# Performance work log

Measured on AMD Instinct MI355X. Metric: run time of the kernel, lower is better.

The kernel has to match this reference:

```python
import jax, jax.numpy as jnp
import numpy as np

D_MODEL = 512
H = 8
D_K = D_MODEL // H


def setup_inputs() -> dict:
    key = jax.random.key(0)
    ks = jax.random.split(key, 11)
    B, S = 2, 4096
    s = 1.0 / np.sqrt(D_MODEL)
    return {
        "q": jax.random.normal(ks[0], (B, S, D_MODEL), jnp.float32),
        "k": jax.random.normal(ks[1], (B, S, D_MODEL), jnp.float32),
        "v": jax.random.normal(ks[2], (B, S, D_MODEL), jnp.float32),
        "w_q": jax.random.normal(ks[3], (D_MODEL, D_MODEL), jnp.float32) * s,
        "b_q": jax.random.normal(ks[4], (D_MODEL,), jnp.float32) * 0.01,
        "w_k": jax.random.normal(ks[5], (D_MODEL, D_MODEL), jnp.float32) * s,
        "b_k": jax.random.normal(ks[6], (D_MODEL,), jnp.float32) * 0.01,
        "w_v": jax.random.normal(ks[7], (D_MODEL, D_MODEL), jnp.float32) * s,
        "b_v": jax.random.normal(ks[8], (D_MODEL,), jnp.float32) * 0.01,
        "w_o": jax.random.normal(ks[9], (D_MODEL, D_MODEL), jnp.float32) * s,
        "b_o": jax.random.normal(ks[10], (D_MODEL,), jnp.float32) * 0.01,
    }


def reference(q, k, v, w_q, b_q, w_k, b_k, w_v, b_v, w_o, b_o):
    B, S, _ = q.shape
    # QKV projections (torch Linear: x @ W.T + b)
    query = q @ w_q.T + b_q
    key_ = k @ w_k.T + b_k
    value = v @ w_v.T + b_v
    # split heads -> [B, H, S, D_K]
    qh = query.reshape(B, S, H, D_K).transpose(0, 2, 1, 3)
    kh = key_.reshape(B, S, H, D_K).transpose(0, 2, 1, 3)
    vh = value.reshape(B, S, H, D_K).transpose(0, 2, 1, 3)
    scores = jnp.einsum('bhsd,bhtd->bhst', qh, kh) / jnp.sqrt(
        jnp.asarray(D_K, qh.dtype))
    attn = jax.nn.softmax(scores, axis=-1)  # dropout = identity in eval
    ctx = jnp.einsum('bhst,bhtd->bhsd', attn, vh)
    out = ctx.transpose(0, 2, 1, 3).reshape(B, S, H * D_K)
    return out @ w_o.T + b_o
```

## Files before the change

### kernel.cpp

```cpp
#include <hip/hip_runtime.h>
#include <hip/hip_bf16.h>


typedef __bf16 bf16_t;
typedef __bf16 bf16x8 __attribute__((ext_vector_type(8)));
typedef __bf16 bf16x4 __attribute__((ext_vector_type(4)));
typedef float f32x4 __attribute__((ext_vector_type(4)));

#define S_LEN 4096
#define NH 8
#define DK 64
#define DMODEL 512
#define NB 2
#define KVB 64
#define QB 128

#define EXP2F(x) __builtin_amdgcn_exp2f(x)

__device__ inline void gload_lds16(const void* g, void* l) {
  __builtin_amdgcn_global_load_lds(
      (const __attribute__((address_space(1))) unsigned int*)g,
      (__attribute__((address_space(3))) unsigned int*)l, 16, 0, 0);
}

__global__ __launch_bounds__(256) void cvt3(
    const float* __restrict__ q, const float* __restrict__ k,
    const float* __restrict__ v, bf16_t* __restrict__ x0,
    bf16_t* __restrict__ x1, bf16_t* __restrict__ x2)
{
  const int z = blockIdx.x >> 11;
  const float* src = z == 0 ? q : z == 1 ? k : v;
  bf16_t* dst = z == 0 ? x0 : z == 1 ? x1 : x2;
  const int i = ((blockIdx.x & 2047) * 256 + threadIdx.x) * 8;
  f32x4 a = *reinterpret_cast<const f32x4*>(src + i);
  f32x4 b = *reinterpret_cast<const f32x4*>(src + i + 4);
  bf16x8 r;
#pragma unroll
  for (int j = 0; j < 4; ++j) { r[j] = (__bf16)a[j]; r[j + 4] = (__bf16)b[j]; }
  *reinterpret_cast<bf16x8*>(dst + i) = r;
}

__global__ __launch_bounds__(256) void cvt_weights(
    const float* __restrict__ w0, const float* __restrict__ w1,
    const float* __restrict__ w2, const float* __restrict__ w3,
    bf16_t* __restrict__ o0, bf16_t* __restrict__ o1,
    bf16_t* __restrict__ o2, bf16_t* __restrict__ o3)
{
  const float* src = blockIdx.y == 0 ? w0 : blockIdx.y == 1 ? w1
                   : blockIdx.y == 2 ? w2 : w3;
  bf16_t* dst = blockIdx.y == 0 ? o0 : blockIdx.y == 1 ? o1
              : blockIdx.y == 2 ? o2 : o3;
  const int i = (blockIdx.x * 256 + threadIdx.x) * 4;
  f32x4 v = *reinterpret_cast<const f32x4*>(src + i);
  bf16x4 r;
#pragma unroll
  for (int j = 0; j < 4; ++j) r[j] = (__bf16)v[j];
  *reinterpret_cast<bf16x4*>(dst + i) = r;
}

template <typename TO, bool FUSED>
__global__ __launch_bounds__(256) void gemm_tile(
    const bf16_t* __restrict__ A0, const bf16_t* __restrict__ W0,
    const float* __restrict__ bb0, TO* __restrict__ oo0,
    const bf16_t* __restrict__ A1, const bf16_t* __restrict__ W1,
    const float* __restrict__ bb1, TO* __restrict__ oo1,
    int mode_last)
{
  const bf16_t* A; const bf16_t* W; const float* bias; TO* out; int mode;
  if (FUSED) {
    if (blockIdx.z == 0) { A = A0; W = W0; bias = bb0; out = oo0; }
    else                 { A = A1; W = W1; bias = bb1; out = oo1; }
    mode = 0;
  } else { A = A0; W = W0; bias = bb0; out = oo0; mode = mode_last; }

  const int mtile = blockIdx.x * 128;
  const int ntile = blockIdx.y * 64;
  const int wave = threadIdx.x >> 6;
  const int lane = threadIdx.x & 63;
  const int l16 = lane & 15;
  const int g = lane >> 4;

  __shared__ bf16_t ldsA[2][128][64];
  __shared__ bf16_t ldsB[2][64][64];

  const int srow8 = 8 * wave + (lane >> 3);
  const int sslot = (lane & 7) ^ ((lane >> 3) & 7);
  const char* Asrc = (const char*)A + ((size_t)(mtile + srow8) * DMODEL) * 2 + sslot * 16;
  const char* Bsrc = (const char*)W + ((size_t)(ntile + srow8) * DMODEL) * 2 + sslot * 16;
  const size_t rblk = (size_t)32 * DMODEL * 2;

  f32x4 acc[2][4];
#pragma unroll
  for (int mb = 0; mb < 2; ++mb)
#pragma unroll
    for (int nb = 0; nb < 4; ++nb) acc[mb][nb] = (f32x4){0.f, 0.f, 0.f, 0.f};

  const int rxor = (l16 & 7) << 4;

#pragma unroll
  for (int c = 0; c < 4; ++c)
    gload_lds16(Asrc + c * rblk, (char*)&ldsA[0][c * 32 + 8 * wave][0]);
#pragma unroll
  for (int c = 0; c < 2; ++c)
    gload_lds16(Bsrc + c * rblk, (char*)&ldsB[0][c * 32 + 8 * wave][0]);
  __syncthreads();

  const int NSTEP = DMODEL / 64;
  int buf = 0;
  for (int t = 0; t < NSTEP; ++t) {
    if (t + 1 < NSTEP) {
      const size_t ko = (size_t)(t + 1) * 128;
#pragma unroll
      for (int c = 0; c < 4; ++c)
        gload_lds16(Asrc + c * rblk + ko, (char*)&ldsA[buf ^ 1][c * 32 + 8 * wave][0]);
#pragma unroll
      for (int c = 0; c < 2; ++c)
        gload_lds16(Bsrc + c * rblk + ko, (char*)&ldsB[buf ^ 1][c * 32 + 8 * wave][0]);
    }

#pragma unroll
    for (int ks = 0; ks < 2; ++ks) {
      bf16x8 af[2];
#pragma unroll
      for (int mb = 0; mb < 2; ++mb) {
        const int arow = wave * 32 + mb * 16 + l16;
        af[mb] = *reinterpret_cast<const bf16x8*>(
            (const char*)&ldsA[buf][0][0] + arow * 128 + ((ks * 64 + g * 16) ^ rxor));
      }
#pragma unroll
      for (int nb = 0; nb < 4; ++nb) {
        const int brow = nb * 16 + l16;
        bf16x8 bfr = *reinterpret_cast<const bf16x8*>(
            (const char*)&ldsB[buf][0][0] + brow * 128 + ((ks * 64 + g * 16) ^ rxor));
#pragma unroll
        for (int mb = 0; mb < 2; ++mb)
          acc[mb][nb] = __builtin_amdgcn_mfma_f32_16x16x32_bf16(af[mb], bfr, acc[mb][nb], 0, 0, 0);
      }
    }

    __syncthreads();
    buf ^= 1;
  }

#pragma unroll
  for (int mb = 0; mb < 2; ++mb) {
    const int m0 = mtile + wave * 32 + mb * 16;
#pragma unroll
    for (int nb = 0; nb < 4; ++nb) {
      const int n = ntile + nb * 16 + l16;
      const float bv = bias[n];
#pragma unroll
      for (int r = 0; r < 4; ++r) {
        const int m = m0 + g * 4 + r;
        float vv = acc[mb][nb][r] + bv;
        size_t addr;
        if (mode == 0) {
          int b = m >> 12, s = m & (S_LEN - 1);
          int h = n >> 6, d = n & 63;
          addr = (((size_t)(b * NH + h) * S_LEN) + s) * DK + d;
        } else if (mode == 2) {
          int b = m >> 12, s = m & (S_LEN - 1);
          int h = n >> 6, d = n & 63;
          addr = (((size_t)(b * NH + h) * DK) + d) * S_LEN + s;
        } else {
          addr = (size_t)m * DMODEL + n;
        }
        out[addr] = (TO)vv;
      }
    }
  }
}

__global__ __launch_bounds__(512) void attn_kernel(
    const bf16_t* __restrict__ Qh, const bf16_t* __restrict__ Kh,
    const bf16_t* __restrict__ Vt, bf16_t* __restrict__ ctx)
{
  const int wg = blockIdx.x;
  const int bh = (wg & 7) * 2 + ((wg >> 3) & 1);
  const int qtile = wg >> 4;
  const int b = bh >> 3, h = bh & 7;
  const int wave = threadIdx.x >> 6;
  const int lane = threadIdx.x & 63;
  const int l16 = lane & 15;
  const int g = lane >> 4;

  __shared__ bf16_t ldsK[2][KVB][64];
  __shared__ bf16_t ldsV[2][KVB][64];
  __shared__ bf16_t pshare[8][16][68];

  const bf16_t* Qp = Qh + (size_t)bh * S_LEN * DK;
  const bf16_t* Kp = Kh + (size_t)bh * S_LEN * DK;
  const bf16_t* Vp = Vt + (size_t)bh * DK * S_LEN;

  const int qrow0 = qtile * QB + wave * 16;

  const int srow = 8 * wave + (lane >> 3);
  const int scol16 = (lane & 7) ^ (lane >> 3);
  const char* Ksrc = (const char*)Kp + (size_t)srow * 128 + scol16 * 16;
  const char* Vsrc = (const char*)Vp + (size_t)srow * (S_LEN * 2) + scol16 * 16;

  const float qscale = 0.125f * 1.44269504089f;
  bf16x8 qf[2];
#pragma unroll
  for (int ks = 0; ks < 2; ++ks) {
    bf16x8 t = *reinterpret_cast<const bf16x8*>(
        Qp + (size_t)(qrow0 + l16) * DK + ks * 32 + g * 8);
#pragma unroll
    for (int j = 0; j < 8; ++j) t[j] = (__bf16)((float)t[j] * qscale);
    qf[ks] = t;
  }

  f32x4 o[4];
#pragma unroll
  for (int db = 0; db < 4; ++db) o[db] = (f32x4){0.f, 0.f, 0.f, 0.f};
  float l_run = 0.f;

  const int rxor = (l16 & 7) << 4;

  gload_lds16(Ksrc, (char*)&ldsK[0][8 * wave][0]);
  gload_lds16(Vsrc, (char*)&ldsV[0][8 * wave][0]);
  __syncthreads();

  const int NT = S_LEN / KVB;

#define TILE_BODY(BUF, T)                                                     \
  {                                                                           \
    const int tt = (T);                                                       \
    if (tt + 1 < NT) {                                                        \
      const size_t koff = (size_t)(tt + 1) * (KVB * 128);                     \
      const size_t voff = (size_t)(tt + 1) * (KVB * 2);                       \
      gload_lds16(Ksrc + koff, (char*)&ldsK[(BUF) ^ 1][8 * wave][0]);         \
      gload_lds16(Vsrc + voff, (char*)&ldsV[(BUF) ^ 1][8 * wave][0]);         \
    }                                                                         \
    f32x4 sc[4];                                                              \
    __builtin_amdgcn_s_setprio(1);                                            \
    _Pragma("unroll")                                                         \
    for (int nb = 0; nb < 4; ++nb) {                                          \
      f32x4 a = (f32x4){0.f, 0.f, 0.f, 0.f};                                  \
      _Pragma("unroll")                                                       \
      for (int ks = 0; ks < 2; ++ks) {                                        \
        const int row = nb * 16 + l16;                                        \
        bf16x8 kf = *reinterpret_cast<const bf16x8*>(                         \
            (const char*)&ldsK[BUF][0][0] + row * 128 +                       \
            ((ks * 64 + g * 16) ^ rxor));                                     \
        a = __builtin_amdgcn_mfma_f32_16x16x32_bf16(kf, qf[ks], a, 0, 0, 0);  \
      }                                                                       \
      sc[nb] = a;                                                             \
    }                                                                         \
    __builtin_amdgcn_s_setprio(0);                                            \
    _Pragma("unroll")                                                         \
    for (int nb = 0; nb < 4; ++nb) {                                          \
      bf16x4 pw;                                                              \
      _Pragma("unroll")                                                       \
      for (int r = 0; r < 4; ++r) {                                           \
        const float p = EXP2F(sc[nb][r]);             \
        l_run += p;                                                           \
        pw[r] = (__bf16)p;                                                    \
      }                                                                       \
      *reinterpret_cast<bf16x4*>(&pshare[wave][l16][nb * 16 + g * 4]) = pw;   \
    }                                                                         \
    __builtin_amdgcn_s_setprio(1);                                            \
    _Pragma("unroll")                                                         \
    for (int ks = 0; ks < 2; ++ks) {                                          \
      bf16x8 pf = *reinterpret_cast<const bf16x8*>(                           \
          &pshare[wave][l16][ks * 32 + g * 8]);                               \
      _Pragma("unroll")                                                       \
      for (int db = 0; db < 4; ++db) {                                        \
        const int row = db * 16 + l16;                                        \
        bf16x8 vf = *reinterpret_cast<const bf16x8*>(                         \
            (const char*)&ldsV[BUF][0][0] + row * 128 +                       \
            ((ks * 64 + g * 16) ^ rxor));                                     \
        o[db] = __builtin_amdgcn_mfma_f32_16x16x32_bf16(vf, pf, o[db], 0, 0, 0); \
      }                                                                       \
    }                                                                         \
    __builtin_amdgcn_s_setprio(0);                                            \
    __syncthreads();                                                          \
  }

  for (int t = 0; t < NT; t += 2) {
    TILE_BODY(0, t)
    TILE_BODY(1, t + 1)
  }
#undef TILE_BODY

  float l_row = l_run;
  l_row += __shfl_xor(l_row, 16);
  l_row += __shfl_xor(l_row, 32);
  const float inv_l = 1.f / l_row;
  bf16_t* crow = ctx + (((size_t)(b * S_LEN + qrow0 + l16)) * NH + h) * DK;
#pragma unroll
  for (int db = 0; db < 4; ++db) {
    bf16x4 cw;
#pragma unroll
    for (int r = 0; r < 4; ++r) cw[r] = (__bf16)(o[db][r] * inv_l);
    *reinterpret_cast<bf16x4*>(crow + db * 16 + g * 4) = cw;
  }
}

extern "C" void kernel_launch(void* const* d_in, const int* in_sizes, int n_in,
                              void* d_out, int out_size, void* d_ws, size_t ws_size,
                              hipStream_t stream)
{
  const float* q   = (const float*)d_in[0];
  const float* k   = (const float*)d_in[1];
  const float* v   = (const float*)d_in[2];
  const float* w_q = (const float*)d_in[3];
  const float* b_q = (const float*)d_in[4];
  const float* w_k = (const float*)d_in[5];
  const float* b_k = (const float*)d_in[6];
  const float* w_v = (const float*)d_in[7];
  const float* b_v = (const float*)d_in[8];
  const float* w_o = (const float*)d_in[9];
  const float* b_o = (const float*)d_in[10];
  float* out = (float*)d_out;

  char* ws = (char*)d_ws;
  const size_t sz = (size_t)NB * NH * S_LEN * DK * sizeof(bf16_t);
  const size_t wsz = (size_t)DMODEL * DMODEL * sizeof(bf16_t);
  bf16_t* X0 = (bf16_t*)(ws);
  bf16_t* X1 = (bf16_t*)(ws + sz);
  bf16_t* X2 = (bf16_t*)(ws + 2 * sz);
  bf16_t* Qh = (bf16_t*)(ws + 3 * sz);
  bf16_t* Kh = (bf16_t*)(ws + 4 * sz);
  bf16_t* Wq = (bf16_t*)(ws + 5 * sz);
  bf16_t* Wk = (bf16_t*)(ws + 5 * sz + wsz);
  bf16_t* Wv = (bf16_t*)(ws + 5 * sz + 2 * wsz);
  bf16_t* Wo = (bf16_t*)(ws + 5 * sz + 3 * wsz);
  bf16_t* Vt  = X0;
  bf16_t* ctx = X1;

  cvt_weights<<<dim3(256, 4), 256, 0, stream>>>(w_q, w_k, w_v, w_o, Wq, Wk, Wv, Wo);
  cvt3<<<dim3(3 * 2048), 256, 0, stream>>>(q, k, v, X0, X1, X2);

  dim3 bb(256);
  gemm_tile<bf16_t, true><<<dim3(64, 8, 2), bb, 0, stream>>>(
      X0, Wq, b_q, Qh, X1, Wk, b_k, Kh, 0);
  gemm_tile<bf16_t, false><<<dim3(64, 8), bb, 0, stream>>>(
      X2, Wv, b_v, Vt, nullptr, nullptr, nullptr, nullptr, 2);

  attn_kernel<<<dim3(512), dim3(512), 0, stream>>>(Qh, Kh, Vt, ctx);

  gemm_tile<float, false><<<dim3(64, 8), bb, 0, stream>>>(
      ctx, Wo, b_o, out, nullptr, nullptr, nullptr, nullptr, 1);
}
```

Before: 149.5 us.

## Process 32 query rows per wave with 4 waves per attention block

The attention kernel now uses 256 threads (4 waves), each handling two 16-row query subtiles, so every K and V fragment read from LDS feeds two MFMAs instead of one. Each wave issues two async global-to-LDS loads per tensor per tile to keep the same 64-row KV tile. This halves LDS read traffic per MFMA and the number of waves contending at barriers. In exchange it raises register pressure (doubled accumulators and Q fragments) and leaves fewer waves to hide latency.

```diff
diff --git a/kernel.cpp b/kernel.cpp
--- a/kernel.cpp
+++ b/kernel.cpp
@@ -171,7 +171,7 @@
   }
 }
 
-__global__ __launch_bounds__(512) void attn_kernel(
+__global__ __launch_bounds__(256) void attn_kernel(
     const bf16_t* __restrict__ Qh, const bf16_t* __restrict__ Kh,
     const bf16_t* __restrict__ Vt, bf16_t* __restrict__ ctx)
 {
@@ -186,39 +186,51 @@
 
   __shared__ bf16_t ldsK[2][KVB][64];
   __shared__ bf16_t ldsV[2][KVB][64];
-  __shared__ bf16_t pshare[8][16][68];
+  __shared__ bf16_t pshare[4][32][68];
 
   const bf16_t* Qp = Qh + (size_t)bh * S_LEN * DK;
   const bf16_t* Kp = Kh + (size_t)bh * S_LEN * DK;
   const bf16_t* Vp = Vt + (size_t)bh * DK * S_LEN;
 
-  const int qrow0 = qtile * QB + wave * 16;
+  const int qrow0 = qtile * QB + wave * 32;
 
   const int srow = 8 * wave + (lane >> 3);
-  const int scol16 = (lane & 7) ^ (lane >> 3);
+  const int scol16 = (lane & 7) ^ ((lane >> 3) & 7);
   const char* Ksrc = (const char*)Kp + (size_t)srow * 128 + scol16 * 16;
   const char* Vsrc = (const char*)Vp + (size_t)srow * (S_LEN * 2) + scol16 * 16;
+  const size_t krow32 = (size_t)32 * 128;
+  const size_t vrow32 = (size_t)32 * (S_LEN * 2);
 
   const float qscale = 0.125f * 1.44269504089f;
-  bf16x8 qf[2];
+  bf16x8 qf0[2], qf1[2];
 #pragma unroll
   for (int ks = 0; ks < 2; ++ks) {
-    bf16x8 t = *reinterpret_cast<const bf16x8*>(
+    bf16x8 t0 = *reinterpret_cast<const bf16x8*>(
         Qp + (size_t)(qrow0 + l16) * DK + ks * 32 + g * 8);
-#pragma unroll
-    for (int j = 0; j < 8; ++j) t[j] = (__bf16)((float)t[j] * qscale);
-    qf[ks] = t;
-  }
-
-  f32x4 o[4];
-#pragma unroll
-  for (int db = 0; db < 4; ++db) o[db] = (f32x4){0.f, 0.f, 0.f, 0.f};
-  float l_run = 0.f;
+    bf16x8 t1 = *reinterpret_cast<const bf16x8*>(
+        Qp + (size_t)(qrow0 + 16 + l16) * DK + ks * 32 + g * 8);
+#pragma unroll
+    for (int j = 0; j < 8; ++j) {
+      t0[j] = (__bf16)((float)t0[j] * qscale);
+      t1[j] = (__bf16)((float)t1[j] * qscale);
+    }
+    qf0[ks] = t0; qf1[ks] = t1;
+  }
+
+  f32x4 o0[4], o1[4];
+#pragma unroll
+  for (int db = 0; db < 4; ++db) {
+    o0[db] = (f32x4){0.f, 0.f, 0.f, 0.f};
+    o1[db] = (f32x4){0.f, 0.f, 0.f, 0.f};
+  }
+  float lr0 = 0.f, lr1 = 0.f;
 
   const int rxor = (l16 & 7) << 4;
 
-  gload_lds16(Ksrc, (char*)&ldsK[0][8 * wave][0]);
+  gload_lds16(Ksrc, (char*)&ldsK[0][srow & 7 ? 8 * wave : 8 * wave][0]);
+  gload_lds16(Ksrc + krow32, (char*)&ldsK[0][32 + 8 * wave][0]);
   gload_lds16(Vsrc, (char*)&ldsV[0][8 * wave][0]);
+  gload_lds16(Vsrc + vrow32, (char*)&ldsV[0][32 + 8 * wave][0]);
   __syncthreads();
 
   const int NT = S_LEN / KVB;
@@ -230,47 +242,60 @@
       const size_t koff = (size_t)(tt + 1) * (KVB * 128);                     \
       const size_t voff = (size_t)(tt + 1) * (KVB * 2);                       \
       gload_lds16(Ksrc + koff, (char*)&ldsK[(BUF) ^ 1][8 * wave][0]);         \
+      gload_lds16(Ksrc + krow32 + koff, (char*)&ldsK[(BUF) ^ 1][32 + 8 * wave][0]); \
       gload_lds16(Vsrc + voff, (char*)&ldsV[(BUF) ^ 1][8 * wave][0]);         \
-    }                                                                         \
-    f32x4 sc[4];                                                              \
+      gload_lds16(Vsrc + vrow32 + voff, (char*)&ldsV[(BUF) ^ 1][32 + 8 * wave][0]); \
+    }                                                                         \
+    f32x4 sc0[4], sc1[4];                                                     \
     __builtin_amdgcn_s_setprio(1);                                            \
     _Pragma("unroll")                                                         \
     for (int nb = 0; nb < 4; ++nb) {                                          \
-      f32x4 a = (f32x4){0.f, 0.f, 0.f, 0.f};                                  \
+      f32x4 a0 = (f32x4){0.f, 0.f, 0.f, 0.f};                                 \
+      f32x4 a1 = (f32x4){0.f, 0.f, 0.f, 0.f};                                 \
       _Pragma("unroll")                                                       \
       for (int ks = 0; ks < 2; ++ks) {                                        \
         const int row = nb * 16 + l16;                                        \
         bf16x8 kf = *reinterpret_cast<const bf16x8*>(                         \
             (const char*)&ldsK[BUF][0][0] + row * 128 +                       \
             ((ks * 64 + g * 16) ^ rxor));                                     \
-        a = __builtin_amdgcn_mfma_f32_16x16x32_bf16(kf, qf[ks], a, 0, 0, 0);  \
+        a0 = __builtin_amdgcn_mfma_f32_16x16x32_bf16(kf, qf0[ks], a0, 0, 0, 0); \
+        a1 = __builtin_amdgcn_mfma_f32_16x16x32_bf16(kf, qf1[ks], a1, 0, 0, 0); \
       }                                                                       \
-      sc[nb] = a;                                                             \
+      sc0[nb] = a0; sc1[nb] = a1;                                             \
     }                                                                         \
     __builtin_amdgcn_s_setprio(0);                                            \
     _Pragma("unroll")                                                         \
     for (int nb = 0; nb < 4; ++nb) {                                          \
-      bf16x4 pw;                                                              \
+      bf16x4 pw0, pw1;                                                        \
       _Pragma("unroll")                                                       \
       for (int r = 0; r < 4; ++r) {                                           \
-        const float p = EXP2F(sc[nb][r]);             \
-        l_run += p;                                                           \
-        pw[r] = (__bf16)p;                                                    \
+        const float p0 = EXP2F(sc0[nb][r]);                                   \
+        const float p1 = EXP2F(sc1[nb][r]);                                   \
+        lr0 += p0; lr1 += p1;                                                 \
+        pw0[r] = (__bf16)p0; pw1[r] = (__bf16)p1;                             \
       }                                                                       \
-      *reinterpret_cast<bf16x4*>(&pshare[wave][l16][nb * 16 + g * 4]) = pw;   \
+      *reinterpret_cast<bf16x4*>(&pshare[wave][l16][nb * 16 + g * 4]) = pw0;  \
+      *reinterpret_cast<bf16x4*>(&pshare[wave][16 + l16][nb * 16 + g * 4]) = pw1; \
+    }                                                                         \
+    bf16x8 pf0[2], pf1[2];                                                    \
+    _Pragma("unroll")                                                         \
+    for (int ks = 0; ks < 2; ++ks) {                                          \
+      pf0[ks] = *reinterpret_cast<const bf16x8*>(                             \
+          &pshare[wave][l16][ks * 32 + g * 8]);                               \
+      pf1[ks] = *reinterpret_cast<const bf16x8*>(                             \
+          &pshare[wave][16 + l16][ks * 32 + g * 8]);                          \
     }                                                                         \
     __builtin_amdgcn_s_setprio(1);                                            \
     _Pragma("unroll")                                                         \
     for (int ks = 0; ks < 2; ++ks) {                                          \
-      bf16x8 pf = *reinterpret_cast<const bf16x8*>(                           \
-          &pshare[wave][l16][ks * 32 + g * 8]);                               \
       _Pragma("unroll")                                                       \
       for (int db = 0; db < 4; ++db) {                                        \
         const int row = db * 16 + l16;                                        \
         bf16x8 vf = *reinterpret_cast<const bf16x8*>(                         \
             (const char*)&ldsV[BUF][0][0] + row * 128 +                       \
             ((ks * 64 + g * 16) ^ rxor));                                     \
-        o[db] = __builtin_amdgcn_mfma_f32_16x16x32_bf16(vf, pf, o[db], 0, 0, 0); \
+        o0[db] = __builtin_amdgcn_mfma_f32_16x16x32_bf16(vf, pf0[ks], o0[db], 0, 0, 0); \
+        o1[db] = __builtin_amdgcn_mfma_f32_16x16x32_bf16(vf, pf1[ks], o1[db], 0, 0, 0); \
       }                                                                       \
     }                                                                         \
     __builtin_amdgcn_s_setprio(0);                                            \
@@ -283,17 +308,22 @@
   }
 #undef TILE_BODY
 
-  float l_row = l_run;
-  l_row += __shfl_xor(l_row, 16);
-  l_row += __shfl_xor(l_row, 32);
-  const float inv_l = 1.f / l_row;
-  bf16_t* crow = ctx + (((size_t)(b * S_LEN + qrow0 + l16)) * NH + h) * DK;
+  float l0 = lr0, l1 = lr1;
+  l0 += __shfl_xor(l0, 16); l0 += __shfl_xor(l0, 32);
+  l1 += __shfl_xor(l1, 16); l1 += __shfl_xor(l1, 32);
+  const float inv0 = 1.f / l0, inv1 = 1.f / l1;
+  bf16_t* crow0 = ctx + (((size_t)(b * S_LEN + qrow0 + l16)) * NH + h) * DK;
+  bf16_t* crow1 = ctx + (((size_t)(b * S_LEN + qrow0 + 16 + l16)) * NH + h) * DK;
 #pragma unroll
   for (int db = 0; db < 4; ++db) {
-    bf16x4 cw;
-#pragma unroll
-    for (int r = 0; r < 4; ++r) cw[r] = (__bf16)(o[db][r] * inv_l);
-    *reinterpret_cast<bf16x4*>(crow + db * 16 + g * 4) = cw;
+    bf16x4 cw0, cw1;
+#pragma unroll
+    for (int r = 0; r < 4; ++r) {
+      cw0[r] = (__bf16)(o0[db][r] * inv0);
+      cw1[r] = (__bf16)(o1[db][r] * inv1);
+    }
+    *reinterpret_cast<bf16x4*>(crow0 + db * 16 + g * 4) = cw0;
+    *reinterpret_cast<bf16x4*>(crow1 + db * 16 + g * 4) = cw1;
   }
 }
 
@@ -338,7 +368,7 @@
   gemm_tile<bf16_t, false><<<dim3(64, 8), bb, 0, stream>>>(
       X2, Wv, b_v, Vt, nullptr, nullptr, nullptr, nullptr, 2);
 
-  attn_kernel<<<dim3(512), dim3(512), 0, stream>>>(Qh, Kh, Vt, ctx);
+  attn_kernel<<<dim3(512), dim3(256), 0, stream>>>(Qh, Kh, Vt, ctx);
 
   gemm_tile<float, false><<<dim3(64, 8), bb, 0, stream>>>(
       ctx, Wo, b_o, out, nullptr, nullptr, nullptr, nullptr, 1);
```

Measured after the change: 155.4 us. 3.9% more time.
